# Kernel tuning notes

Hardware: AMD Instinct MI355X
Metric: run time of the kernel (lower is better)

Reference implementation:

```python
import jax, jax.numpy as jnp
import numpy as np

B, C, H, W = 4, 256, 64, 64
E = C // 8  # embedding_channels = inChannels // k


def setup_inputs() -> dict:
    key = jax.random.key(0)
    ks = jax.random.split(key, 9)
    sc = 1.0 / np.sqrt(C)
    so = 1.0 / np.sqrt(E)
    return {
        "x": jax.random.normal(ks[0], (B, C, H, W), dtype=jnp.float32),
        "Wk": jax.random.normal(ks[1], (E, C), dtype=jnp.float32) * sc,
        "bk": jax.random.normal(ks[2], (E,), dtype=jnp.float32) * 0.01,
        "Wq": jax.random.normal(ks[3], (E, C), dtype=jnp.float32) * sc,
        "bq": jax.random.normal(ks[4], (E,), dtype=jnp.float32) * 0.01,
        "Wv": jax.random.normal(ks[5], (E, C), dtype=jnp.float32) * sc,
        "bv": jax.random.normal(ks[6], (E,), dtype=jnp.float32) * 0.01,
        "Wo": jax.random.normal(ks[7], (C, E), dtype=jnp.float32) * so,
        "bo": jax.random.normal(ks[8], (C,), dtype=jnp.float32) * 0.01,
    }


def reference(x, Wk, bk, Wq, bq, Wv, bv, Wo, bo):
    b, c, h, w = x.shape
    n = h * w
    gamma = jnp.float32(0.5)  # non-learned branch (learned=False default)

    def conv1x1(inp, Wt, bt):
        # 1x1 conv == channel-mixing matmul: [b,c,h,w] x [e,c] -> [b,e,h,w]
        return jnp.einsum('bchw,ec->behw', inp, Wt) + bt[None, :, None, None]

    f = conv1x1(x, Wk, bk).reshape(b, -1, n)  # key   [b,E,N]
    g = conv1x1(x, Wq, bq).reshape(b, -1, n)  # query [b,E,N]
    hx = conv1x1(x, Wv, bv).reshape(b, -1, n)  # value [b,E,N]

    s = jnp.einsum('bei,bej->bij', f, g)       # f^T @ g, [b,N,N]
    beta = jax.nn.softmax(s, axis=1)           # softmax over dim 1 (rows) as in torch
    v = jnp.einsum('bei,bij->bej', hx, beta)   # h @ beta, [b,E,N]
    v = v.reshape(b, -1, h, w)

    o = jnp.einsum('behw,ce->bchw', v, Wo) + bo[None, :, None, None]
    y = gamma * o + x
    return y, o, gamma
```

## Files before the change

kernel.cpp:

```cpp
#include <hip/hip_runtime.h>

#define B_ 4
#define C_ 256
#define N_ 4096
#define E_ 32

typedef _Float16 f16x8 __attribute__((ext_vector_type(8)));
typedef _Float16 f16x4 __attribute__((ext_vector_type(4)));
typedef _Float16 f16x2 __attribute__((ext_vector_type(2)));
typedef float f32x4 __attribute__((ext_vector_type(4)));
typedef float f32x2 __attribute__((ext_vector_type(2)));

#define LOG2E 1.44269504088896f

__global__ __launch_bounds__(256) void proj_kernel(
    const float* __restrict__ x,
    const float* __restrict__ Wk, const float* __restrict__ bk,
    const float* __restrict__ Wq, const float* __restrict__ bq,
    const float* __restrict__ Wv, const float* __restrict__ bv,
    _Float16* __restrict__ Qb, _Float16* __restrict__ Kb, _Float16* __restrict__ Vb)
{
    const int m   = blockIdx.x >> 8;
    const int rem = blockIdx.x & 255;
    const int b   = rem >> 6;
    const int n0  = (rem & 63) << 6;
    const int t    = threadIdx.x;
    const int lane = t & 63;
    const int wave = t >> 6;
    const int l15  = lane & 15;
    const int quad = lane >> 4;

    __shared__ _Float16 xT[64][264];
    __shared__ _Float16 Wl[32][264];

    const float* W    = (m == 0) ? Wk : (m == 1) ? Wq : Wv;
    const float* bias = (m == 0) ? bk : (m == 1) ? bq : bv;

    for (int i4 = t; i4 < (E_ * C_) / 4; i4 += 256) {
        float4 wv = ((const float4*)W)[i4];
        int e = (i4 * 4) >> 8, c = (i4 * 4) & 255;
        f16x4 tp = {(_Float16)wv.x, (_Float16)wv.y, (_Float16)wv.z, (_Float16)wv.w};
        *(f16x4*)&Wl[e][c] = tp;
    }
    for (int i4 = t; i4 < (64 * 256) / 4; i4 += 256) {
        int j4 = (i4 & 15) * 4;
        int c  = i4 >> 4;
        float4 xv = *(const float4*)(x + (size_t)(b * C_ + c) * N_ + n0 + j4);
        xT[j4 + 0][c] = (_Float16)xv.x;
        xT[j4 + 1][c] = (_Float16)xv.y;
        xT[j4 + 2][c] = (_Float16)xv.z;
        xT[j4 + 3][c] = (_Float16)xv.w;
    }
    __syncthreads();

    f16x8 Bf[8];
    for (int kk = 0; kk < 8; ++kk)
        Bf[kk] = *(const f16x8*)&xT[wave * 16 + l15][kk * 32 + quad * 8];

    const float sc = (m == 1) ? LOG2E : 1.0f;
    for (int et = 0; et < 2; ++et) {
        f32x4 acc = {0.f, 0.f, 0.f, 0.f};
        for (int kk = 0; kk < 8; ++kk) {
            f16x8 Af = *(const f16x8*)&Wl[et * 16 + l15][kk * 32 + quad * 8];
            acc = __builtin_amdgcn_mfma_f32_16x16x32_f16(Af, Bf[kk], acc, 0, 0, 0);
        }
        const int n = n0 + wave * 16 + l15;
        for (int r = 0; r < 4; ++r) {
            const int e = et * 16 + quad * 4 + r;
            float v = (acc[r] + bias[e]) * sc;
            _Float16 hv = (_Float16)v;
            if      (m == 0) Kb[(size_t)(b * N_ + n) * E_ + e] = hv;
            else if (m == 1) Qb[(size_t)(b * N_ + n) * E_ + e] = hv;
            else             Vb[(size_t)(b * E_ + e) * N_ + n] = hv;
        }
    }
}

__global__ __launch_bounds__(256, 4) void attn_kernel(
    const _Float16* __restrict__ Qb, const _Float16* __restrict__ Kb,
    const _Float16* __restrict__ Vb, _Float16* __restrict__ Ob)
{
    const int wave = threadIdx.x >> 6;
    const int lane = threadIdx.x & 63;
    const int l15  = lane & 15, quad = lane >> 4;
    const int jg   = blockIdx.x;
    const int b    = jg >> 8;
    const int j0   = (jg & 255) << 4;

    __shared__ _Float16 pb[4][16][136];
    __shared__ float    osum[4][16][36];
    __shared__ float    mls[4][2][16];

    f16x8 Qf = *(const f16x8*)(Qb + (size_t)(b * N_ + j0 + l15) * E_ + quad * 8);

    f32x4 O0 = {0, 0, 0, 0}, O1 = {0, 0, 0, 0};
    float mrow = -1e30f, lsum = 0.f;

    const _Float16* Kbase = Kb + (size_t)b * N_ * E_;
    const _Float16* Vbase = Vb + (size_t)b * E_ * N_;
    const int ibase = wave << 10;

    f16x8 Kf[8];
    for (int s = 0; s < 8; ++s)
        Kf[s] = *(const f16x8*)(Kbase + (size_t)(ibase + s * 16 + l15) * E_ + quad * 8);

    for (int it = 0; it < 8; ++it) {
        const int i0 = ibase + it * 128;
        f32x4 S[8];
        for (int s = 0; s < 8; ++s) {
            f32x4 z = {0, 0, 0, 0};
            S[s] = __builtin_amdgcn_mfma_f32_16x16x32_f16(Kf[s], Qf, z, 0, 0, 0);
        }
        float mx = -1e30f;
        for (int s = 0; s < 8; ++s)
            for (int r = 0; r < 4; ++r) mx = fmaxf(mx, S[s][r]);
        mx = fmaxf(mx, __shfl_xor(mx, 16));
        mx = fmaxf(mx, __shfl_xor(mx, 32));
        float mnew  = fmaxf(mrow, mx);
        float alpha = exp2f(mrow - mnew);
        mrow = mnew;
        float ps = 0.f;
        for (int s = 0; s < 8; ++s)
            for (int r = 0; r < 4; ++r) {
                float p = exp2f(S[s][r] - mnew);
                S[s][r] = p;
                ps += p;
            }
        lsum = lsum * alpha + ps;
        for (int r = 0; r < 4; ++r) { O0[r] *= alpha; O1[r] *= alpha; }
        for (int s = 0; s < 8; ++s) {
            f16x4 tp = {(_Float16)S[s][0], (_Float16)S[s][1],
                        (_Float16)S[s][2], (_Float16)S[s][3]};
            *(f16x4*)&pb[wave][l15][s * 16 + quad * 4] = tp;
        }
        asm volatile("s_waitcnt lgkmcnt(0)" ::: "memory");
        f16x8 P[4];
        for (int kc = 0; kc < 4; ++kc)
            P[kc] = *(const f16x8*)&pb[wave][l15][kc * 32 + quad * 8];
        f16x8 Va[4], Vc[4];
        for (int kc = 0; kc < 4; ++kc) {
            Va[kc] = *(const f16x8*)(Vbase + (size_t)l15 * N_ + i0 + kc * 32 + quad * 8);
            Vc[kc] = *(const f16x8*)(Vbase + (size_t)(16 + l15) * N_ + i0 + kc * 32 + quad * 8);
        }
        const int inext = (it < 7) ? (i0 + 128) : ibase;
        for (int s = 0; s < 8; ++s)
            Kf[s] = *(const f16x8*)(Kbase + (size_t)(inext + s * 16 + l15) * E_ + quad * 8);
        for (int kc = 0; kc < 4; ++kc) {
            O0 = __builtin_amdgcn_mfma_f32_16x16x32_f16(Va[kc], P[kc], O0, 0, 0, 0);
            O1 = __builtin_amdgcn_mfma_f32_16x16x32_f16(Vc[kc], P[kc], O1, 0, 0, 0);
        }
    }

    lsum += __shfl_xor(lsum, 16);
    lsum += __shfl_xor(lsum, 32);
    if (quad == 0) { mls[wave][0][l15] = mrow; mls[wave][1][l15] = lsum; }
    __syncthreads();

    float M = -1e30f, ms[4], ls[4];
    for (int s = 0; s < 4; ++s) {
        ms[s] = mls[s][0][l15]; ls[s] = mls[s][1][l15];
        M = fmaxf(M, ms[s]);
    }
    float L = 0.f;
    for (int s = 0; s < 4; ++s) L += ls[s] * exp2f(ms[s] - M);
    const float w = exp2f(mrow - M) / L;

    *(f32x4*)&osum[wave][l15][quad * 4]      = O0 * w;
    *(f32x4*)&osum[wave][l15][16 + quad * 4] = O1 * w;
    __syncthreads();

    const int j  = threadIdx.x >> 4;
    const int e2 = (threadIdx.x & 15) * 2;
    float a0 = 0.f, a1 = 0.f;
    for (int s = 0; s < 4; ++s) {
        f32x2 v = *(const f32x2*)&osum[s][j][e2];
        a0 += v[0]; a1 += v[1];
    }
    f16x2 o2 = {(_Float16)a0, (_Float16)a1};
    *(f16x2*)(Ob + (size_t)(b * N_ + j0 + j) * E_ + e2) = o2;
}

__global__ __launch_bounds__(256) void out_kernel(
    const _Float16* __restrict__ Ob, const float* __restrict__ Wo,
    const float* __restrict__ bo, const float* __restrict__ x,
    float* __restrict__ out)
{
    const int bi  = blockIdx.x;
    const int b   = bi >> 8;
    const int rem = bi & 255;
    const int n0  = (rem >> 2) << 6;
    const int cq  = rem & 3;
    const int t = threadIdx.x, lane = t & 63, wave = t >> 6;
    const int l15 = lane & 15, quad = lane >> 4;

    __shared__ _Float16 Wl[64][40];
    for (int i4 = t; i4 < (64 * E_) / 4; i4 += 256) {
        int c = (i4 * 4) >> 5, e = (i4 * 4) & 31;
        float4 wv = *(const float4*)(Wo + (size_t)(cq * 64 + c) * E_ + e);
        f16x4 tp = {(_Float16)wv.x, (_Float16)wv.y, (_Float16)wv.z, (_Float16)wv.w};
        *(f16x4*)&Wl[c][e] = tp;
    }
    __syncthreads();

    const int nloc = wave * 16 + l15;
    f16x8 Bf = *(const f16x8*)(Ob + (size_t)(b * N_ + n0 + nloc) * E_ + quad * 8);

    float* out_y = out;
    float* out_o = out + (size_t)B_ * C_ * N_;

    for (int tt = 0; tt < 4; ++tt) {
        f16x8 Af = *(const f16x8*)&Wl[tt * 16 + l15][quad * 8];
        f32x4 z = {0, 0, 0, 0};
        f32x4 acc = __builtin_amdgcn_mfma_f32_16x16x32_f16(Af, Bf, z, 0, 0, 0);
        for (int r = 0; r < 4; ++r) {
            const int c = cq * 64 + tt * 16 + quad * 4 + r;
            size_t idx = (size_t)(b * C_ + c) * N_ + n0 + nloc;
            float ov = acc[r] + bo[c];
            out_o[idx] = ov;
            out_y[idx] = 0.5f * ov + x[idx];
        }
    }
    if (bi == 0 && t == 0)
        out[(size_t)2 * B_ * C_ * N_] = 0.5f;
}

extern "C" void kernel_launch(void* const* d_in, const int* in_sizes, int n_in,
                              void* d_out, int out_size, void* d_ws, size_t ws_size,
                              hipStream_t stream)
{
    const float* x  = (const float*)d_in[0];
    const float* Wk = (const float*)d_in[1];
    const float* bk = (const float*)d_in[2];
    const float* Wq = (const float*)d_in[3];
    const float* bq = (const float*)d_in[4];
    const float* Wv = (const float*)d_in[5];
    const float* bv = (const float*)d_in[6];
    const float* Wo = (const float*)d_in[7];
    const float* bo = (const float*)d_in[8];
    float* out = (float*)d_out;

    char* ws = (char*)d_ws;
    _Float16* Qb = (_Float16*)(ws);
    _Float16* Kb = (_Float16*)(ws + (1u << 20));
    _Float16* Vb = (_Float16*)(ws + (2u << 20));
    _Float16* Ob = (_Float16*)(ws + (3u << 20));

    proj_kernel<<<dim3(3 * B_ * (N_ / 64)), dim3(256), 0, stream>>>(
        x, Wk, bk, Wq, bq, Wv, bv, Qb, Kb, Vb);
    attn_kernel<<<dim3(B_ * (N_ / 16)), dim3(256), 0, stream>>>(
        Qb, Kb, Vb, Ob);
    out_kernel <<<dim3(4 * B_ * (N_ / 64)), dim3(256), 0, stream>>>(
        Ob, Wo, bo, x, out);
}
```

Measured before the change: 151.4 us.

## Split attention keys across eight waves per block instead of four

The attention kernel now launches 512 threads per block, and each of the eight waves handles 512 keys instead of 1024. This doubles the number of resident waves, so memory and MFMA latency are better hidden at the same grid size. The per-wave row max and sum reductions are rewritten as balanced trees to expose more instruction-level parallelism. Shared memory is one aliased buffer holding both the P staging tiles and the cross-wave output partials, and the final merge now combines eight partials. The tighter launch bound may cap registers and cause spills, and the merge step does more work.

```diff
diff --git a/kernel.cpp b/kernel.cpp
--- a/kernel.cpp
+++ b/kernel.cpp
@@ -76,7 +76,7 @@
     }
 }
 
-__global__ __launch_bounds__(256, 4) void attn_kernel(
+__global__ __launch_bounds__(512, 8) void attn_kernel(
     const _Float16* __restrict__ Qb, const _Float16* __restrict__ Kb,
     const _Float16* __restrict__ Vb, _Float16* __restrict__ Ob)
 {
@@ -87,9 +87,10 @@
     const int b    = jg >> 8;
     const int j0   = (jg & 255) << 4;
 
-    __shared__ _Float16 pb[4][16][136];
-    __shared__ float    osum[4][16][36];
-    __shared__ float    mls[4][2][16];
+    __shared__ __align__(16) char smem[8 * 4352];
+    __shared__ float mls[8][2][16];
+
+    _Float16 (*pb)[136] = (_Float16 (*)[136])(smem + wave * 4352);
 
     f16x8 Qf = *(const f16x8*)(Qb + (size_t)(b * N_ + j0 + l15) * E_ + quad * 8);
 
@@ -98,51 +99,63 @@
 
     const _Float16* Kbase = Kb + (size_t)b * N_ * E_;
     const _Float16* Vbase = Vb + (size_t)b * E_ * N_;
-    const int ibase = wave << 10;
+    const int ibase = wave << 9;
 
     f16x8 Kf[8];
     for (int s = 0; s < 8; ++s)
         Kf[s] = *(const f16x8*)(Kbase + (size_t)(ibase + s * 16 + l15) * E_ + quad * 8);
 
-    for (int it = 0; it < 8; ++it) {
+    for (int it = 0; it < 4; ++it) {
         const int i0 = ibase + it * 128;
         f32x4 S[8];
         for (int s = 0; s < 8; ++s) {
             f32x4 z = {0, 0, 0, 0};
             S[s] = __builtin_amdgcn_mfma_f32_16x16x32_f16(Kf[s], Qf, z, 0, 0, 0);
         }
-        float mx = -1e30f;
-        for (int s = 0; s < 8; ++s)
-            for (int r = 0; r < 4; ++r) mx = fmaxf(mx, S[s][r]);
+        float t0, t1, t2, t3;
+        t0 = fmaxf(fmaxf(S[0][0], S[0][1]), fmaxf(S[0][2], S[0][3]));
+        t1 = fmaxf(fmaxf(S[1][0], S[1][1]), fmaxf(S[1][2], S[1][3]));
+        t2 = fmaxf(fmaxf(S[2][0], S[2][1]), fmaxf(S[2][2], S[2][3]));
+        t3 = fmaxf(fmaxf(S[3][0], S[3][1]), fmaxf(S[3][2], S[3][3]));
+        float mA = fmaxf(fmaxf(t0, t1), fmaxf(t2, t3));
+        t0 = fmaxf(fmaxf(S[4][0], S[4][1]), fmaxf(S[4][2], S[4][3]));
+        t1 = fmaxf(fmaxf(S[5][0], S[5][1]), fmaxf(S[5][2], S[5][3]));
+        t2 = fmaxf(fmaxf(S[6][0], S[6][1]), fmaxf(S[6][2], S[6][3]));
+        t3 = fmaxf(fmaxf(S[7][0], S[7][1]), fmaxf(S[7][2], S[7][3]));
+        float mx = fmaxf(mA, fmaxf(fmaxf(t0, t1), fmaxf(t2, t3)));
         mx = fmaxf(mx, __shfl_xor(mx, 16));
         mx = fmaxf(mx, __shfl_xor(mx, 32));
         float mnew  = fmaxf(mrow, mx);
         float alpha = exp2f(mrow - mnew);
         mrow = mnew;
-        float ps = 0.f;
-        for (int s = 0; s < 8; ++s)
-            for (int r = 0; r < 4; ++r) {
-                float p = exp2f(S[s][r] - mnew);
-                S[s][r] = p;
-                ps += p;
-            }
+        float ss[8];
+        for (int s = 0; s < 8; ++s) {
+            float p0 = exp2f(S[s][0] - mnew);
+            float p1 = exp2f(S[s][1] - mnew);
+            float p2 = exp2f(S[s][2] - mnew);
+            float p3 = exp2f(S[s][3] - mnew);
+            S[s][0] = p0; S[s][1] = p1; S[s][2] = p2; S[s][3] = p3;
+            ss[s] = (p0 + p1) + (p2 + p3);
+        }
+        float ps = ((ss[0] + ss[1]) + (ss[2] + ss[3]))
+                 + ((ss[4] + ss[5]) + (ss[6] + ss[7]));
         lsum = lsum * alpha + ps;
         for (int r = 0; r < 4; ++r) { O0[r] *= alpha; O1[r] *= alpha; }
         for (int s = 0; s < 8; ++s) {
             f16x4 tp = {(_Float16)S[s][0], (_Float16)S[s][1],
                         (_Float16)S[s][2], (_Float16)S[s][3]};
-            *(f16x4*)&pb[wave][l15][s * 16 + quad * 4] = tp;
+            *(f16x4*)&pb[l15][s * 16 + quad * 4] = tp;
         }
         asm volatile("s_waitcnt lgkmcnt(0)" ::: "memory");
         f16x8 P[4];
         for (int kc = 0; kc < 4; ++kc)
-            P[kc] = *(const f16x8*)&pb[wave][l15][kc * 32 + quad * 8];
+            P[kc] = *(const f16x8*)&pb[l15][kc * 32 + quad * 8];
         f16x8 Va[4], Vc[4];
         for (int kc = 0; kc < 4; ++kc) {
             Va[kc] = *(const f16x8*)(Vbase + (size_t)l15 * N_ + i0 + kc * 32 + quad * 8);
             Vc[kc] = *(const f16x8*)(Vbase + (size_t)(16 + l15) * N_ + i0 + kc * 32 + quad * 8);
         }
-        const int inext = (it < 7) ? (i0 + 128) : ibase;
+        const int inext = (it < 3) ? (i0 + 128) : ibase;
         for (int s = 0; s < 8; ++s)
             Kf[s] = *(const f16x8*)(Kbase + (size_t)(inext + s * 16 + l15) * E_ + quad * 8);
         for (int kc = 0; kc < 4; ++kc) {
@@ -156,28 +169,26 @@
     if (quad == 0) { mls[wave][0][l15] = mrow; mls[wave][1][l15] = lsum; }
     __syncthreads();
 
-    float M = -1e30f, ms[4], ls[4];
-    for (int s = 0; s < 4; ++s) {
+    float M = -1e30f, ms[8], ls[8];
+    for (int s = 0; s < 8; ++s) {
         ms[s] = mls[s][0][l15]; ls[s] = mls[s][1][l15];
         M = fmaxf(M, ms[s]);
     }
     float L = 0.f;
-    for (int s = 0; s < 4; ++s) L += ls[s] * exp2f(ms[s] - M);
+    for (int s = 0; s < 8; ++s) L += ls[s] * exp2f(ms[s] - M);
     const float w = exp2f(mrow - M) / L;
 
-    *(f32x4*)&osum[wave][l15][quad * 4]      = O0 * w;
-    *(f32x4*)&osum[wave][l15][16 + quad * 4] = O1 * w;
-    __syncthreads();
-
-    const int j  = threadIdx.x >> 4;
-    const int e2 = (threadIdx.x & 15) * 2;
-    float a0 = 0.f, a1 = 0.f;
-    for (int s = 0; s < 4; ++s) {
-        f32x2 v = *(const f32x2*)&osum[s][j][e2];
-        a0 += v[0]; a1 += v[1];
-    }
-    f16x2 o2 = {(_Float16)a0, (_Float16)a1};
-    *(f16x2*)(Ob + (size_t)(b * N_ + j0 + j) * E_ + e2) = o2;
+    float (*osum)[36] = (float (*)[36])(smem + wave * 2304);
+    *(f32x4*)&osum[l15][quad * 4]      = O0 * w;
+    *(f32x4*)&osum[l15][16 + quad * 4] = O1 * w;
+    __syncthreads();
+
+    const int j = threadIdx.x >> 5;
+    const int e = threadIdx.x & 31;
+    float a = 0.f;
+    for (int s = 0; s < 8; ++s)
+        a += ((const float (*)[36])(smem + s * 2304))[j][e];
+    Ob[(size_t)(b * N_ + j0 + j) * E_ + e] = (_Float16)a;
 }
 
 __global__ __launch_bounds__(256) void out_kernel(
@@ -247,7 +258,7 @@
 
     proj_kernel<<<dim3(3 * B_ * (N_ / 64)), dim3(256), 0, stream>>>(
         x, Wk, bk, Wq, bq, Wv, bv, Qb, Kb, Vb);
-    attn_kernel<<<dim3(B_ * (N_ / 16)), dim3(256), 0, stream>>>(
+    attn_kernel<<<dim3(B_ * (N_ / 16)), dim3(512), 0, stream>>>(
         Qb, Kb, Vb, Ob);
     out_kernel <<<dim3(4 * B_ * (N_ / 64)), dim3(256), 0, stream>>>(
         Ob, Wo, bo, x, out);
```

Result: slower. 185.0 us (+22.2%).
